# Optimization experiments

Hardware: AMD Instinct MI355X
Metric: run time of the kernel (lower is better)

The kernel has to match this reference:

```python
import jax, jax.numpy as jnp
import numpy as np

LMAX = 8                         # lmax-1 used by s2/so3 irreps
DIMS = [2 * l + 1 for l in range(LMAX + 1)]
S2_OFF = np.cumsum([0] + DIMS).tolist()            # offsets into 81-dim s2 irreps
SO3_OFF = np.cumsum([0] + [d * d for d in DIMS]).tolist()  # offsets into 969-dim so3 irreps
S2_DIM = S2_OFF[-1]              # 81
SO3_DIM = SO3_OFF[-1]            # 969
F_IN = 81                        # multiplicity into S2Conv
F_SO3 = 300
C = 768                          # encoder feature channels
KS = 7                           # encoder feature map / kernel size
B = 8
G_S2 = 48                        # s2 healpix grid rec_level=1
G_ACT = 4096                     # SO3Activation grid points (stand-in for res=20 grid)
G_SO3 = 36864                    # so3 healpix grid rec_level=3


def setup_inputs() -> dict:
    key = jax.random.key(0)
    ks = jax.random.split(key, 7)
    return {
        "x": jax.random.normal(ks[0], (B, C, KS, KS), jnp.float32),
        "F": jax.random.normal(ks[1], (F_IN, S2_DIM * C, KS, KS), jnp.float32) * 0.02,
        "w_s2": jax.random.normal(ks[2], (F_IN, F_SO3, G_S2), jnp.float32) * 0.1,
        "Y": jax.random.normal(ks[3], (G_S2, S2_DIM), jnp.float32),
        "w_so3": jax.random.normal(ks[4], (F_SO3, 1, G_SO3), jnp.float32) * 0.1,
        "D": jax.random.normal(ks[5], (G_SO3, SO3_DIM), jnp.float32),
        "D_act": jax.random.normal(ks[6], (G_ACT, SO3_DIM), jnp.float32),
    }


def _forward(x, F, w_s2, Y, w_so3, D, D_act):
    b = x.shape[0]
    # ---- Induction layer: split expanded R2Conv filter into 768-channel chunks,
    # stack, contract with feature map. g_split: (n=81, c_out=81, C, 7, 7)
    g = jnp.swapaxes(F.reshape(F_IN, S2_DIM, C, KS, KS), 0, 1)
    y = jnp.einsum('ijkhw,akhw->aji', g, x)          # (B, 81, 81): (batch, f_in, s2 irreps)

    # ---- S2Conv: expand kernel into irrep space, per-l block linear (s2 -> so3 irreps)
    psi = jnp.einsum('ni,xyn->xyi', Y, w_s2) / np.sqrt(G_S2)  # (81, 300, 81)
    outs = []
    for l, d in enumerate(DIMS):
        o = S2_OFF[l]
        xl = y[:, :, o:o + d]                        # (B, f_in, 2l+1)
        wl = psi[:, :, o:o + d]                      # (f_in, f_out, mul_out=2l+1)
        ol = jnp.einsum('bfm,fgu->bgum', xl, wl) / np.sqrt(F_IN)
        outs.append(ol.reshape(b, F_SO3, d * d))
    z = jnp.concatenate(outs, axis=-1)               # (B, 300, 969)

    # ---- SO3Activation: to grid, relu, back to irreps
    s = jnp.einsum('bfi,gi->bfg', z, D_act)
    z = jnp.einsum('bfg,gi->bfi', jax.nn.relu(s), D_act) / G_ACT

    # ---- SO3Conv: expand kernel via Wigner-D buffer, per-l block linear (so3 -> so3)
    psi2 = jnp.einsum('ni,xyn->xyi', D, w_so3) / np.sqrt(G_SO3)  # (300, 1, 969)
    outs = []
    for l, d in enumerate(DIMS):
        o = SO3_OFF[l]
        xl = z[:, :, o:o + d * d].reshape(b, F_SO3, d, d)   # (B, f, u, m)
        wl = psi2[:, :, o:o + d * d].reshape(F_SO3, 1, d, d)  # (f, g, v, u)
        ol = jnp.einsum('bfum,fgvu->bgvm', xl, wl) / np.sqrt(F_SO3 * d)
        outs.append(ol.reshape(b, 1, d * d))
    return jnp.concatenate(outs, axis=-1)            # (B, 1, 969)


def reference(x, F, w_s2, Y, w_so3, D, D_act):
    return _forward(x, F, w_s2, Y, w_so3, D, D_act)
```

## Files before the change

kernel.cpp:

```cpp
#include <hip/hip_runtime.h>
#include <hip/hip_bf16.h>
#include <math.h>

#define THREADS 256

constexpr int B_    = 8;
constexpr int C_    = 768;
constexpr int KS_   = 7;
constexpr int F_IN  = 81;
constexpr int F_SO3 = 300;
constexpr int S2_DIM  = 81;
constexpr int SO3_DIM = 969;
constexpr int G_S2  = 48;
constexpr int G_ACT = 4096;
constexpr int G_SO3 = 36864;
constexpr int CKK   = C_ * KS_ * KS_;
constexpr int CKK4  = CKK / 4;
constexpr int NPAIR = F_IN * S2_DIM;

constexpr int D2_SPLIT = 4;
constexpr int E1_SPLIT = 16;
constexpr int F_SPLIT  = 5;

__constant__ int d_S2_OFF[10]  = {0, 1, 4, 9, 16, 25, 36, 49, 64, 81};
__constant__ int d_SO3_OFF[10] = {0, 1, 10, 35, 84, 165, 286, 455, 680, 969};

struct CEnt { unsigned char u, m, so, l; };
struct CLut { CEnt v[992]; };
constexpr CLut make_clut() {
  CLut t{};
  int S2O[10]  = {0, 1, 4, 9, 16, 25, 36, 49, 64, 81};
  int SO3O[10] = {0, 1, 10, 35, 84, 165, 286, 455, 680, 969};
  for (int i = 0; i < 969; ++i) {
    int l = 0;
    while (i >= SO3O[l + 1]) ++l;
    int d = 2 * l + 1, r = i - SO3O[l];
    t.v[i].u  = (unsigned char)(r / d);
    t.v[i].m  = (unsigned char)(r % d);
    t.v[i].so = (unsigned char)S2O[l];
    t.v[i].l  = (unsigned char)l;
  }
  return t;
}
__constant__ CLut g_clut = make_clut();

using short8 = __attribute__((ext_vector_type(8))) short;
using f32x4  = __attribute__((ext_vector_type(4))) float;
using f4v    = __attribute__((ext_vector_type(4))) float;

#define GL16(gp, lp)                                                        \
  __builtin_amdgcn_global_load_lds(                                         \
      (const __attribute__((address_space(1))) void*)(gp),                  \
      (__attribute__((address_space(3))) void*)(lp), 16, 0, 0)

constexpr size_t AL(size_t x) { return (x + 1023) & ~(size_t)1023; }
constexpr size_t O_Y     = 0;
constexpr size_t O_PSI   = O_Y     + AL((size_t)8 * NPAIR * 4);
constexpr size_t O_ZBF   = O_PSI   + AL((size_t)F_IN * F_SO3 * 81 * 4);
constexpr size_t O_DACT  = O_ZBF   + AL((size_t)2432 * 1024 * 2);
constexpr size_t O_DACTT = O_DACT  + AL((size_t)4096 * 1024 * 2);
constexpr size_t O_WSO3  = O_DACTT + AL((size_t)1024 * 4096 * 2);
constexpr size_t O_DT    = O_WSO3  + AL((size_t)384 * 36864 * 2);
constexpr size_t O_SBF   = O_DT    + AL((size_t)1024 * 36864 * 2);
constexpr size_t O_D2P   = O_SBF   + AL((size_t)2432 * 4096 * 2);
constexpr size_t O_E1P   = O_D2P   + AL((size_t)D2_SPLIT * 2432 * 1024 * 4);
constexpr size_t O_PSI2  = O_E1P   + AL((size_t)E1_SPLIT * 384 * 1024 * 4);
constexpr size_t O_SFP   = O_PSI2  + AL((size_t)F_SO3 * SO3_DIM * 4);
constexpr size_t FAST_NEED = O_SFP + AL((size_t)F_SPLIT * 8 * SO3_DIM * 4);

constexpr size_t WS_Y    = 0;
constexpr size_t WS_PSI  = 52488;
constexpr size_t WS_Z    = 2020788;
constexpr size_t WS_S    = 4346388;
constexpr size_t WS_Z2   = 14176788;
constexpr size_t WS_P2P  = 16502388;
constexpr size_t WS_PSI2 = 18827988;

__global__ __launch_bounds__(THREADS) void k_stage_a3(
    const float* __restrict__ Fm, const float* __restrict__ x, float* __restrict__ y) {
  const int p0  = blockIdx.x * 3;
  const int tid = threadIdx.x;
  const f4v* __restrict__ F4 = (const f4v*)Fm;
  const f4v* __restrict__ x4 = (const f4v*)x;

  float acc[3][8];
#pragma unroll
  for (int p = 0; p < 3; ++p)
#pragma unroll
    for (int b = 0; b < 8; ++b) acc[p][b] = 0.f;

  for (int i = tid; i < CKK4; i += THREADS) {
    f4v xv[8];
#pragma unroll
    for (int b = 0; b < 8; ++b) xv[b] = x4[b * CKK4 + i];
#pragma unroll
    for (int p = 0; p < 3; ++p) {
      f4v fv = __builtin_nontemporal_load(&F4[(size_t)(p0 + p) * CKK4 + i]);
#pragma unroll
      for (int b = 0; b < 8; ++b)
        acc[p][b] += fv[0] * xv[b][0] + fv[1] * xv[b][1] + fv[2] * xv[b][2] + fv[3] * xv[b][3];
    }
  }

  __shared__ float red[4][24];
  const int lane = tid & 63, wid = tid >> 6;
#pragma unroll
  for (int p = 0; p < 3; ++p) {
#pragma unroll
    for (int b = 0; b < 8; ++b) {
      float v = acc[p][b];
      v += __shfl_down(v, 32);
      v += __shfl_down(v, 16);
      v += __shfl_down(v, 8);
      v += __shfl_down(v, 4);
      v += __shfl_down(v, 2);
      v += __shfl_down(v, 1);
      if (lane == 0) red[wid][p * 8 + b] = v;
    }
  }
  __syncthreads();
  if (tid < 24) {
    float v = red[0][tid] + red[1][tid] + red[2][tid] + red[3][tid];
    int p = tid / 8, b = tid % 8;
    y[(size_t)b * NPAIR + p0 + p] = v;
  }
}

__device__ __forceinline__ void cvt_body(const float* __restrict__ src,
                                         __hip_bfloat16* __restrict__ dst,
                                         int R, int Cs, int Cp, int blk) {
  size_t idx = (size_t)blk * THREADS + threadIdx.x;
  int r = (int)(idx / (unsigned)Cp), c = (int)(idx % (unsigned)Cp);
  float v = (r < R && c < Cs) ? src[(size_t)r * Cs + c] : 0.f;
  dst[idx] = __float2bfloat16(v);
}

__device__ __forceinline__ void tr_body(const float* __restrict__ src,
                                        __hip_bfloat16* __restrict__ dst,
                                        int R, int Cs, size_t dstStride, int bx, int by) {
  __shared__ float tile[32][33];
  const int c0 = bx * 32, r0 = by * 32;
  const int tx = threadIdx.x & 31, ty = threadIdx.x >> 5;
#pragma unroll
  for (int i = 0; i < 32; i += 8) {
    int r = r0 + ty + i, c = c0 + tx;
    tile[ty + i][tx] = (r < R && c < Cs) ? src[(size_t)r * Cs + c] : 0.f;
  }
  __syncthreads();
#pragma unroll
  for (int i = 0; i < 32; i += 8) {
    int c = c0 + ty + i, r = r0 + tx;
    if (c < Cs && r < R) dst[(size_t)c * dstStride + r] = __float2bfloat16(tile[tx][ty + i]);
  }
}

__device__ __forceinline__ void psi_body(const float* __restrict__ w_s2,
                                         const float* __restrict__ Y,
                                         float* __restrict__ psi, int blk) {
  int idx = blk * THREADS + threadIdx.x;
  if (idx >= F_IN * F_SO3 * S2_DIM) return;
  int s  = idx % S2_DIM;
  int fg = idx / S2_DIM;
  const float* w = w_s2 + (size_t)fg * G_S2;
  float acc = 0.f;
#pragma unroll 8
  for (int n = 0; n < G_S2; ++n) acc += w[n] * Y[n * S2_DIM + s];
  psi[idx] = acc * 0.14433756729740643f;
}

constexpr int UB1 = 16384;
constexpr int UB2 = 3968;
constexpr int UB3 = 55296;
constexpr int UB4 = 35712;
constexpr int UB5 = 7689;
constexpr int UB_TOT = UB1 + UB2 + UB3 + UB4 + UB5;

__global__ __launch_bounds__(THREADS) void k_uber(
    const float* __restrict__ D_act, __hip_bfloat16* __restrict__ Dact_bf,
    __hip_bfloat16* __restrict__ DactT_bf,
    const float* __restrict__ w_so3, __hip_bfloat16* __restrict__ wso3_bf,
    const float* __restrict__ D, __hip_bfloat16* __restrict__ DT_bf,
    const float* __restrict__ w_s2, const float* __restrict__ Y, float* __restrict__ psi) {
  int b = blockIdx.x;
  if (b < UB1) { cvt_body(D_act, Dact_bf, G_ACT, SO3_DIM, 1024, b); return; }
  b -= UB1;
  if (b < UB2) { tr_body(D_act, DactT_bf, G_ACT, SO3_DIM, 4096, b % 31, b / 31); return; }
  b -= UB2;
  if (b < UB3) { cvt_body(w_so3, wso3_bf, F_SO3, G_SO3, G_SO3, b); return; }
  b -= UB3;
  if (b < UB4) { tr_body(D, DT_bf, G_SO3, SO3_DIM, 36864, b % 31, b / 31); return; }
  b -= UB4;
  psi_body(w_s2, Y, psi, b);
}

__global__ __launch_bounds__(THREADS) void k_stage_c_bf(
    const float* __restrict__ y, const float* __restrict__ psi, __hip_bfloat16* __restrict__ z) {
  const int b = blockIdx.x / F_SO3;
  const int g = blockIdx.x % F_SO3;
  __shared__ float ybl[NPAIR];
  __shared__ float psl[NPAIR];
  const int tid = threadIdx.x;
  for (int t = tid; t < NPAIR; t += THREADS) {
    ybl[t] = y[(size_t)b * NPAIR + t];
    int f = t / S2_DIM, s = t % S2_DIM;
    psl[t] = psi[((size_t)f * F_SO3 + g) * S2_DIM + s];
  }
  __syncthreads();
  for (int i = tid; i < 1024; i += THREADS) {
    float acc = 0.f;
    if (i < SO3_DIM) {
      CEnt e = g_clut.v[i];
      int im = e.so + e.m, iu = e.so + e.u;
#pragma unroll 9
      for (int f = 0; f < F_IN; ++f)
        acc += ybl[f * S2_DIM + im] * psl[f * S2_DIM + iu];
      acc *= (1.0f / 9.0f);
    }
    z[((size_t)b * F_SO3 + g) * 1024 + i] = __float2bfloat16(acc);
  }
}

struct GemmDesc {
  const __hip_bfloat16* A;
  const __hip_bfloat16* B;
  void* C;
  int K, kSpan, Ncols;
  float scale;
  size_t splitStride;
  int gx, gy, gz, epi;
};

__device__ __forceinline__ void mfma_nt_body(const GemmDesc g, unsigned lin) {
  __shared__ __align__(16) char smem[32768];
  char* As = smem;
  char* Bs = smem + 16384;

  unsigned nwg = (unsigned)(g.gx * g.gy * g.gz);
  if ((nwg & 7u) == 0u) {
    unsigned q = nwg >> 3;
    lin = (lin & 7u) * q + (lin >> 3);
  }
  const int bxi = (int)(lin % (unsigned)g.gx);
  const unsigned t1 = lin / (unsigned)g.gx;
  const int byi = (int)(t1 % (unsigned)g.gy);
  const int bzi = (int)(t1 / (unsigned)g.gy);

  const int t    = threadIdx.x;
  const int lane = t & 63;
  const int wave = t >> 6;
  const int wr   = wave >> 1, wc = wave & 1;
  const int bm = byi * 128, bn = bxi * 128;
  const int kBegin = bzi * g.kSpan;
  const int kEnd   = kBegin + g.kSpan;

  const char* pA[4];
  const char* pB[4];
  int ldsOff[4];
#pragma unroll
  for (int i = 0; i < 4; ++i) {
    int L   = i * 4096 + t * 16;
    int row = L >> 7;
    int kb  = (L & 127) ^ ((row & 7) << 4);
    pA[i] = (const char*)g.A + ((size_t)(bm + row) * g.K) * 2 + kb;
    pB[i] = (const char*)g.B + ((size_t)(bn + row) * g.K) * 2 + kb;
    ldsOff[i] = L;
  }

  f32x4 acc[4][4] = {};

  for (int k0 = kBegin; k0 < kEnd; k0 += 64) {
    size_t koff = (size_t)k0 * 2;
#pragma unroll
    for (int i = 0; i < 4; ++i) {
      GL16(pA[i] + koff, As + ldsOff[i]);
      GL16(pB[i] + koff, Bs + ldsOff[i]);
    }
    __syncthreads();
#pragma unroll
    for (int kk = 0; kk < 2; ++kk) {
      const int klin = kk * 64 + ((lane >> 4) << 4);
      short8 af[4], bfr[4];
#pragma unroll
      for (int m = 0; m < 4; ++m) {
        int ra = (wr << 6) + (m << 4) + (lane & 15);
        af[m] = *(const short8*)(As + ra * 128 + (klin ^ ((ra & 7) << 4)));
        int rb = (wc << 6) + (m << 4) + (lane & 15);
        bfr[m] = *(const short8*)(Bs + rb * 128 + (klin ^ ((rb & 7) << 4)));
      }
#pragma unroll
      for (int m = 0; m < 4; ++m)
#pragma unroll
        for (int n = 0; n < 4; ++n)
          acc[m][n] = __builtin_amdgcn_mfma_f32_16x16x32_bf16(af[m], bfr[n], acc[m][n], 0, 0, 0);
    }
    __syncthreads();
  }

  const int rbase = bm + (wr << 6) + ((lane >> 4) << 2);
  const int cbase = bn + (wc << 6) + (lane & 15);
  if (g.epi == 0) {
    float* C = (float*)g.C + (size_t)bzi * g.splitStride;
#pragma unroll
    for (int m = 0; m < 4; ++m)
#pragma unroll
      for (int n = 0; n < 4; ++n)
#pragma unroll
        for (int r = 0; r < 4; ++r)
          C[(size_t)(rbase + m * 16 + r) * g.Ncols + (cbase + n * 16)] = acc[m][n][r] * g.scale;
  } else {
    __hip_bfloat16* C = (__hip_bfloat16*)g.C;
#pragma unroll
    for (int m = 0; m < 4; ++m)
#pragma unroll
      for (int n = 0; n < 4; ++n)
#pragma unroll
        for (int r = 0; r < 4; ++r)
          C[(size_t)(rbase + m * 16 + r) * g.Ncols + (cbase + n * 16)] =
              __float2bfloat16(fmaxf(acc[m][n][r], 0.f));
  }
}

__global__ __launch_bounds__(THREADS) void k_mfma_dual(GemmDesc g0, GemmDesc g1, int n0) {
  if ((int)blockIdx.x < n0) mfma_nt_body(g0, blockIdx.x);
  else                      mfma_nt_body(g1, blockIdx.x - n0);
}

__global__ __launch_bounds__(THREADS) void k_mfma_reduce(
    GemmDesc g, int n0,
    const float* __restrict__ parts, float* __restrict__ dst, int R, int C,
    size_t rowStride, size_t splitStride, size_t dstStride, int nSplit, float scale) {
  if ((int)blockIdx.x < n0) { mfma_nt_body(g, blockIdx.x); return; }
  int idx = (int)(blockIdx.x - n0) * THREADS + threadIdx.x;
  if (idx >= R * C) return;
  int r = idx / C, c = idx % C;
  float a = 0.f;
  for (int s = 0; s < nSplit; ++s) a += parts[(size_t)s * splitStride + (size_t)r * rowStride + c];
  dst[(size_t)r * dstStride + c] = a * scale;
}

__global__ __launch_bounds__(THREADS) void k_stage_f_part(
    const float* __restrict__ d2p, const float* __restrict__ psi2, float* __restrict__ partial) {
  const int b  = blockIdx.x / 9;
  const int l  = blockIdx.x % 9;
  const int sp = blockIdx.y;
  const int d = 2 * l + 1, d2 = d * d;
  const int off = d_SO3_OFF[l];
  constexpr size_t SS = (size_t)2432 * 1024;
  __shared__ float zb[10][289];
  __shared__ float pb[10][289];
  const int tid = threadIdx.x;
  float acc[2] = {0.f, 0.f};
  const int fBeg = sp * (F_SO3 / F_SPLIT), fEnd = fBeg + F_SO3 / F_SPLIT;
  for (int fc = fBeg; fc < fEnd; fc += 10) {
    for (int t = tid; t < 10 * d2; t += THREADS) {
      int fl = t / d2, q = t - fl * d2;
      int f  = fc + fl;
      size_t zi = ((size_t)b * F_SO3 + f) * 1024 + off + q;
      float zv = d2p[zi] + d2p[zi + SS] + d2p[zi + 2 * SS] + d2p[zi + 3 * SS];
      zb[fl][q] = zv * (1.0f / G_ACT);
      pb[fl][q] = psi2[(size_t)f * SO3_DIM + off + q];
    }
    __syncthreads();
#pragma unroll 2
    for (int io = 0; io < 2; ++io) {
      int i = tid + io * THREADS;
      if (i < d2) {
        int v = i / d, m = i - v * d;
        float a = acc[io];
#pragma unroll
        for (int fl = 0; fl < 10; ++fl) {
          float s_ = 0.f;
          for (int u = 0; u < d; ++u)
            s_ += zb[fl][u * d + m] * pb[fl][v * d + u];
          a += s_;
        }
        acc[io] = a;
      }
    }
    __syncthreads();
  }
  for (int io = 0; io < 2; ++io) {
    int i = tid + io * THREADS;
    if (i < d2) partial[((size_t)sp * 8 + b) * SO3_DIM + off + i] = acc[io];
  }
}

__global__ __launch_bounds__(THREADS) void k_stage_f_red(
    const float* __restrict__ partial, float* __restrict__ out) {
  int idx = blockIdx.x * THREADS + threadIdx.x;
  if (idx >= 8 * SO3_DIM) return;
  int b = idx / SO3_DIM, i = idx % SO3_DIM;
  int l = g_clut.v[i].l;
  float a = 0.f;
#pragma unroll
  for (int sp = 0; sp < F_SPLIT; ++sp)
    a += partial[((size_t)sp * 8 + b) * SO3_DIM + i];
  out[(size_t)b * SO3_DIM + i] = a * rsqrtf(300.0f * (float)(2 * l + 1));
}

__global__ __launch_bounds__(THREADS) void k_psi(
    const float* __restrict__ w_s2, const float* __restrict__ Y, float* __restrict__ psi) {
  psi_body(w_s2, Y, psi, blockIdx.x);
}

__global__ __launch_bounds__(THREADS) void k_stage_c(
    const float* __restrict__ y, const float* __restrict__ psi, float* __restrict__ z) {
  const int b = blockIdx.x / F_SO3;
  const int g = blockIdx.x % F_SO3;
  __shared__ float ybl[NPAIR];
  __shared__ float psl[NPAIR];
  const int tid = threadIdx.x;
  for (int t = tid; t < NPAIR; t += THREADS) {
    ybl[t] = y[(size_t)b * NPAIR + t];
    int f = t / S2_DIM, s = t % S2_DIM;
    psl[t] = psi[((size_t)f * F_SO3 + g) * S2_DIM + s];
  }
  __syncthreads();
  for (int i = tid; i < SO3_DIM; i += THREADS) {
    CEnt e = g_clut.v[i];
    int im = e.so + e.m, iu = e.so + e.u;
    float acc = 0.f;
#pragma unroll 9
    for (int f = 0; f < F_IN; ++f)
      acc += ybl[f * S2_DIM + im] * psl[f * S2_DIM + iu];
    z[((size_t)b * F_SO3 + g) * SO3_DIM + i] = acc * (1.0f / 9.0f);
  }
}

__global__ __launch_bounds__(THREADS) void k_gemm_nt_relu(
    const float* __restrict__ A, const float* __restrict__ Bm, float* __restrict__ Cm,
    int M, int N, int K) {
  __shared__ float As[16][68];
  __shared__ float Bs[16][68];
  const int bm = blockIdx.y * 64, bn = blockIdx.x * 64;
  const int t  = threadIdx.x;
  const int lk = t & 15, lm = t >> 4;
  const int tn = t & 15, tm = t >> 4;
  float acc[4][4] = {};
  for (int k0 = 0; k0 < K; k0 += 16) {
    int gk = k0 + lk;
#pragma unroll
    for (int j = 0; j < 4; ++j) {
      int m  = lm + 16 * j;
      int gm = bm + m;
      As[lk][m] = (gm < M && gk < K) ? A[(size_t)gm * K + gk] : 0.f;
      int gn = bn + m;
      Bs[lk][m] = (gn < N && gk < K) ? Bm[(size_t)gn * K + gk] : 0.f;
    }
    __syncthreads();
#pragma unroll
    for (int k = 0; k < 16; ++k) {
      float4 av = *(const float4*)&As[k][tm * 4];
      float4 bv = *(const float4*)&Bs[k][tn * 4];
      float a[4] = {av.x, av.y, av.z, av.w};
      float bb[4] = {bv.x, bv.y, bv.z, bv.w};
#pragma unroll
      for (int i2 = 0; i2 < 4; ++i2)
#pragma unroll
        for (int j2 = 0; j2 < 4; ++j2)
          acc[i2][j2] += a[i2] * bb[j2];
    }
    __syncthreads();
  }
#pragma unroll
  for (int i2 = 0; i2 < 4; ++i2) {
    int gm = bm + tm * 4 + i2;
    if (gm >= M) continue;
#pragma unroll
    for (int j2 = 0; j2 < 4; ++j2) {
      int gn = bn + tn * 4 + j2;
      if (gn < N) Cm[(size_t)gm * N + gn] = fmaxf(acc[i2][j2], 0.f);
    }
  }
}

__global__ __launch_bounds__(THREADS) void k_gemm_nn(
    const float* __restrict__ A, const float* __restrict__ Bm, float* __restrict__ Cm,
    int M, int N, int K, int kSpan, float scale, size_t cStride) {
  __shared__ float As[16][68];
  __shared__ float Bs[16][68];
  const int bm = blockIdx.y * 64, bn = blockIdx.x * 64;
  const int t   = threadIdx.x;
  const int lk  = t & 15, lm = t >> 4;
  const int ln  = t & 63, lkq = t >> 6;
  const int tn  = t & 15, tm = t >> 4;
  const int kBegin = blockIdx.z * kSpan;
  const int kEnd   = kBegin + kSpan;
  float* C = Cm + (size_t)blockIdx.z * cStride;
  float acc[4][4] = {};
  for (int k0 = kBegin; k0 < kEnd; k0 += 16) {
    {
      int gk = k0 + lk;
#pragma unroll
      for (int j = 0; j < 4; ++j) {
        int m = lm + 16 * j, gm = bm + m;
        As[lk][m] = (gm < M) ? A[(size_t)gm * K + gk] : 0.f;
      }
    }
    {
      int gn = bn + ln;
#pragma unroll
      for (int j = 0; j < 4; ++j) {
        int k = lkq + 4 * j;
        Bs[k][ln] = (gn < N) ? Bm[(size_t)(k0 + k) * N + gn] : 0.f;
      }
    }
    __syncthreads();
#pragma unroll
    for (int k = 0; k < 16; ++k) {
      float4 av = *(const float4*)&As[k][tm * 4];
      float4 bv = *(const float4*)&Bs[k][tn * 4];
      float a[4] = {av.x, av.y, av.z, av.w};
      float bb[4] = {bv.x, bv.y, bv.z, bv.w};
#pragma unroll
      for (int i2 = 0; i2 < 4; ++i2)
#pragma unroll
        for (int j2 = 0; j2 < 4; ++j2)
          acc[i2][j2] += a[i2] * bb[j2];
    }
    __syncthreads();
  }
#pragma unroll
  for (int i2 = 0; i2 < 4; ++i2) {
    int gm = bm + tm * 4 + i2;
    if (gm >= M) continue;
#pragma unroll
    for (int j2 = 0; j2 < 4; ++j2) {
      int gn = bn + tn * 4 + j2;
      if (gn < N) C[(size_t)gm * N + gn] = acc[i2][j2] * scale;
    }
  }
}

__global__ __launch_bounds__(THREADS) void k_reduce_psi2(
    const float* __restrict__ parts, float* __restrict__ psi2) {
  int idx = blockIdx.x * THREADS + threadIdx.x;
  if (idx >= F_SO3 * SO3_DIM) return;
  float acc = 0.f;
#pragma unroll
  for (int s = 0; s < 8; ++s) acc += parts[(size_t)s * (F_SO3 * SO3_DIM) + idx];
  psi2[idx] = acc * (1.0f / 192.0f);
}

__global__ __launch_bounds__(THREADS) void k_stage_f(
    const float* __restrict__ z2, const float* __restrict__ psi2, float* __restrict__ out,
    int zStride) {
  const int b = blockIdx.x / 9;
  const int l = blockIdx.x % 9;
  const int d = 2 * l + 1, d2 = d * d;
  const int off = d_SO3_OFF[l];
  __shared__ float zb[10][289];
  __shared__ float pb[10][289];
  const int tid = threadIdx.x;
  float acc[2] = {0.f, 0.f};
  const float scale = rsqrtf(300.0f * (float)d);
  for (int fc = 0; fc < F_SO3; fc += 10) {
    for (int t = tid; t < 10 * d2; t += THREADS) {
      int fl = t / d2, q = t - fl * d2;
      int f  = fc + fl;
      zb[fl][q] = z2[((size_t)b * F_SO3 + f) * zStride + off + q];
      pb[fl][q] = psi2[(size_t)f * SO3_DIM + off + q];
    }
    __syncthreads();
#pragma unroll 2
    for (int io = 0; io < 2; ++io) {
      int i = tid + io * THREADS;
      if (i < d2) {
        int v = i / d, m = i - v * d;
        float a = acc[io];
#pragma unroll
        for (int fl = 0; fl < 10; ++fl) {
          float s_ = 0.f;
          for (int u = 0; u < d; ++u)
            s_ += zb[fl][u * d + m] * pb[fl][v * d + u];
          a += s_;
        }
        acc[io] = a;
      }
    }
    __syncthreads();
  }
  for (int io = 0; io < 2; ++io) {
    int i = tid + io * THREADS;
    if (i < d2) out[(size_t)b * SO3_DIM + off + i] = acc[io] * scale;
  }
}

extern "C" void kernel_launch(void* const* d_in, const int* in_sizes, int n_in,
                              void* d_out, int out_size, void* d_ws, size_t ws_size,
                              hipStream_t stream) {
  const float* x     = (const float*)d_in[0];
  const float* Fm    = (const float*)d_in[1];
  const float* w_s2  = (const float*)d_in[2];
  const float* Y     = (const float*)d_in[3];
  const float* w_so3 = (const float*)d_in[4];
  const float* D     = (const float*)d_in[5];
  const float* D_act = (const float*)d_in[6];
  float* out = (float*)d_out;

  if (ws_size >= FAST_NEED) {
    char* p = (char*)d_ws;
    float*          y       = (float*)(p + O_Y);
    float*          psi     = (float*)(p + O_PSI);
    __hip_bfloat16* z_bf    = (__hip_bfloat16*)(p + O_ZBF);
    __hip_bfloat16* Dact_bf = (__hip_bfloat16*)(p + O_DACT);
    __hip_bfloat16* DactT_bf= (__hip_bfloat16*)(p + O_DACTT);
    __hip_bfloat16* wso3_bf = (__hip_bfloat16*)(p + O_WSO3);
    __hip_bfloat16* DT_bf   = (__hip_bfloat16*)(p + O_DT);
    __hip_bfloat16* s_bf    = (__hip_bfloat16*)(p + O_SBF);
    float*          d2p     = (float*)(p + O_D2P);
    float*          e1p     = (float*)(p + O_E1P);
    float*          psi2    = (float*)(p + O_PSI2);
    float*          sfp     = (float*)(p + O_SFP);

    k_stage_a3<<<NPAIR / 3, THREADS, 0, stream>>>(Fm, x, y);
    k_uber<<<UB_TOT, THREADS, 0, stream>>>(
        D_act, Dact_bf, DactT_bf, w_so3, wso3_bf, D, DT_bf, w_s2, Y, psi);
    k_stage_c_bf<<<B_ * F_SO3, THREADS, 0, stream>>>(y, psi, z_bf);

    GemmDesc e1{wso3_bf, DT_bf, e1p, G_SO3, G_SO3 / E1_SPLIT, 1024, 1.f,
                (size_t)384 * 1024, 8, 3, E1_SPLIT, 0};
    GemmDesc d1{z_bf, Dact_bf, s_bf, 1024, 1024, 4096, 1.f, 0, 32, 19, 1, 1};
    int nE1 = 8 * 3 * E1_SPLIT;
    int nD1 = 32 * 19;
    k_mfma_dual<<<nE1 + nD1, THREADS, 0, stream>>>(e1, d1, nE1);

    GemmDesc d2{s_bf, DactT_bf, d2p, 4096, 4096 / D2_SPLIT, 1024, 1.f,
                (size_t)2432 * 1024, 8, 19, D2_SPLIT, 0};
    int nD2 = 8 * 19 * D2_SPLIT;
    int nE1r = (F_SO3 * SO3_DIM + THREADS - 1) / THREADS;
    k_mfma_reduce<<<nD2 + nE1r, THREADS, 0, stream>>>(
        d2, nD2, e1p, psi2, F_SO3, SO3_DIM, 1024, (size_t)384 * 1024, SO3_DIM,
        E1_SPLIT, 1.0f / 192.0f);

    k_stage_f_part<<<dim3(B_ * 9, F_SPLIT), THREADS, 0, stream>>>(d2p, psi2, sfp);
    k_stage_f_red<<<(8 * SO3_DIM + THREADS - 1) / THREADS, THREADS, 0, stream>>>(sfp, out);
  } else {
    float* ws  = (float*)d_ws;
    float* y    = ws + WS_Y;
    float* psi  = ws + WS_PSI;
    float* z    = ws + WS_Z;
    float* s    = ws + WS_S;
    float* z2   = ws + WS_Z2;
    float* p2p  = ws + WS_P2P;
    float* psi2 = ws + WS_PSI2;

    k_stage_a3<<<NPAIR / 3, THREADS, 0, stream>>>(Fm, x, y);
    k_psi<<<(F_IN * F_SO3 * S2_DIM + THREADS - 1) / THREADS, THREADS, 0, stream>>>(w_s2, Y, psi);
    k_stage_c<<<B_ * F_SO3, THREADS, 0, stream>>>(y, psi, z);
    k_gemm_nt_relu<<<dim3(G_ACT / 64, (B_ * F_SO3 + 63) / 64), THREADS, 0, stream>>>(
        z, D_act, s, B_ * F_SO3, G_ACT, SO3_DIM);
    k_gemm_nn<<<dim3((SO3_DIM + 63) / 64, (B_ * F_SO3 + 63) / 64, 1), THREADS, 0, stream>>>(
        s, D_act, z2, B_ * F_SO3, SO3_DIM, G_ACT, G_ACT, 1.0f / G_ACT, 0);
    k_gemm_nn<<<dim3((SO3_DIM + 63) / 64, (F_SO3 + 63) / 64, 8), THREADS, 0, stream>>>(
        w_so3, D, p2p, F_SO3, SO3_DIM, G_SO3, G_SO3 / 8, 1.0f, (size_t)F_SO3 * SO3_DIM);
    k_reduce_psi2<<<(F_SO3 * SO3_DIM + THREADS - 1) / THREADS, THREADS, 0, stream>>>(p2p, psi2);
    k_stage_f<<<B_ * 9, THREADS, 0, stream>>>(z2, psi2, out, SO3_DIM);
  }
}
```

Before: 611.0 us.

## Regroup independent stages into fused launches to overlap stage A, C and GEMMs

```diff
diff --git a/kernel.cpp b/kernel.cpp
--- a/kernel.cpp
+++ b/kernel.cpp
@@ -76,9 +76,10 @@
 constexpr size_t WS_P2P  = 16502388;
 constexpr size_t WS_PSI2 = 18827988;
 
-__global__ __launch_bounds__(THREADS) void k_stage_a3(
-    const float* __restrict__ Fm, const float* __restrict__ x, float* __restrict__ y) {
-  const int p0  = blockIdx.x * 3;
+__device__ __forceinline__ void stage_a_body(
+    const float* __restrict__ Fm, const float* __restrict__ x, float* __restrict__ y,
+    char* smemc, int blk) {
+  const int p0  = blk * 3;
   const int tid = threadIdx.x;
   const f4v* __restrict__ F4 = (const f4v*)Fm;
   const f4v* __restrict__ x4 = (const f4v*)x;
@@ -102,7 +103,7 @@
     }
   }
 
-  __shared__ float red[4][24];
+  float (*red)[24] = (float(*)[24])smemc;
   const int lane = tid & 63, wid = tid >> 6;
 #pragma unroll
   for (int p = 0; p < 3; ++p) {
@@ -137,8 +138,9 @@
 
 __device__ __forceinline__ void tr_body(const float* __restrict__ src,
                                         __hip_bfloat16* __restrict__ dst,
-                                        int R, int Cs, size_t dstStride, int bx, int by) {
-  __shared__ float tile[32][33];
+                                        int R, int Cs, size_t dstStride, int bx, int by,
+                                        char* smemc) {
+  float (*tile)[33] = (float(*)[33])smemc;
   const int c0 = bx * 32, r0 = by * 32;
   const int tx = threadIdx.x & 31, ty = threadIdx.x >> 5;
 #pragma unroll
@@ -168,37 +170,43 @@
   psi[idx] = acc * 0.14433756729740643f;
 }
 
+constexpr int PA  = NPAIR / 3;
 constexpr int UB1 = 16384;
 constexpr int UB2 = 3968;
 constexpr int UB3 = 55296;
 constexpr int UB4 = 35712;
 constexpr int UB5 = 7689;
-constexpr int UB_TOT = UB1 + UB2 + UB3 + UB4 + UB5;
-
-__global__ __launch_bounds__(THREADS) void k_uber(
+constexpr int PREP_TOT = PA + UB1 + UB2 + UB3 + UB4 + UB5;
+
+__global__ __launch_bounds__(THREADS) void k_prep(
+    const float* __restrict__ Fm, const float* __restrict__ x, float* __restrict__ y,
     const float* __restrict__ D_act, __hip_bfloat16* __restrict__ Dact_bf,
     __hip_bfloat16* __restrict__ DactT_bf,
     const float* __restrict__ w_so3, __hip_bfloat16* __restrict__ wso3_bf,
     const float* __restrict__ D, __hip_bfloat16* __restrict__ DT_bf,
     const float* __restrict__ w_s2, const float* __restrict__ Y, float* __restrict__ psi) {
+  __shared__ __align__(16) char smem[4352];
   int b = blockIdx.x;
+  if (b < PA) { stage_a_body(Fm, x, y, smem, b); return; }
+  b -= PA;
   if (b < UB1) { cvt_body(D_act, Dact_bf, G_ACT, SO3_DIM, 1024, b); return; }
   b -= UB1;
-  if (b < UB2) { tr_body(D_act, DactT_bf, G_ACT, SO3_DIM, 4096, b % 31, b / 31); return; }
+  if (b < UB2) { tr_body(D_act, DactT_bf, G_ACT, SO3_DIM, 4096, b % 31, b / 31, smem); return; }
   b -= UB2;
   if (b < UB3) { cvt_body(w_so3, wso3_bf, F_SO3, G_SO3, G_SO3, b); return; }
   b -= UB3;
-  if (b < UB4) { tr_body(D, DT_bf, G_SO3, SO3_DIM, 36864, b % 31, b / 31); return; }
+  if (b < UB4) { tr_body(D, DT_bf, G_SO3, SO3_DIM, 36864, b % 31, b / 31, smem); return; }
   b -= UB4;
   psi_body(w_s2, Y, psi, b);
 }
 
-__global__ __launch_bounds__(THREADS) void k_stage_c_bf(
-    const float* __restrict__ y, const float* __restrict__ psi, __hip_bfloat16* __restrict__ z) {
-  const int b = blockIdx.x / F_SO3;
-  const int g = blockIdx.x % F_SO3;
-  __shared__ float ybl[NPAIR];
-  __shared__ float psl[NPAIR];
+__device__ __forceinline__ void stage_c_body(
+    const float* __restrict__ y, const float* __restrict__ psi, __hip_bfloat16* __restrict__ z,
+    char* smemc, int blk) {
+  const int b = blk / F_SO3;
+  const int g = blk % F_SO3;
+  float* ybl = (float*)smemc;
+  float* psl = ybl + 6592;
   const int tid = threadIdx.x;
   for (int t = tid; t < NPAIR; t += THREADS) {
     ybl[t] = y[(size_t)b * NPAIR + t];
@@ -230,8 +238,7 @@
   int gx, gy, gz, epi;
 };
 
-__device__ __forceinline__ void mfma_nt_body(const GemmDesc g, unsigned lin) {
-  __shared__ __align__(16) char smem[32768];
+__device__ __forceinline__ void mfma_nt_body(const GemmDesc g, unsigned lin, char* smem) {
   char* As = smem;
   char* Bs = smem + 16384;
 
@@ -320,22 +327,31 @@
   }
 }
 
-__global__ __launch_bounds__(THREADS) void k_mfma_dual(GemmDesc g0, GemmDesc g1, int n0) {
-  if ((int)blockIdx.x < n0) mfma_nt_body(g0, blockIdx.x);
-  else                      mfma_nt_body(g1, blockIdx.x - n0);
-}
-
-__global__ __launch_bounds__(THREADS) void k_mfma_reduce(
-    GemmDesc g, int n0,
+__global__ __launch_bounds__(THREADS) void k_e1_c(
+    GemmDesc e1, int nE1,
+    const float* __restrict__ y, const float* __restrict__ psi, __hip_bfloat16* __restrict__ z) {
+  __shared__ __align__(16) char smem[52672];
+  if ((int)blockIdx.x < nE1) mfma_nt_body(e1, blockIdx.x, smem);
+  else                       stage_c_body(y, psi, z, smem, blockIdx.x - nE1);
+}
+
+__global__ __launch_bounds__(THREADS) void k_d1_e1r(
+    GemmDesc d1, int n0,
     const float* __restrict__ parts, float* __restrict__ dst, int R, int C,
     size_t rowStride, size_t splitStride, size_t dstStride, int nSplit, float scale) {
-  if ((int)blockIdx.x < n0) { mfma_nt_body(g, blockIdx.x); return; }
+  __shared__ __align__(16) char smem[32768];
+  if ((int)blockIdx.x < n0) { mfma_nt_body(d1, blockIdx.x, smem); return; }
   int idx = (int)(blockIdx.x - n0) * THREADS + threadIdx.x;
   if (idx >= R * C) return;
   int r = idx / C, c = idx % C;
   float a = 0.f;
   for (int s = 0; s < nSplit; ++s) a += parts[(size_t)s * splitStride + (size_t)r * rowStride + c];
   dst[(size_t)r * dstStride + c] = a * scale;
+}
+
+__global__ __launch_bounds__(THREADS) void k_mfma_single(GemmDesc g) {
+  __shared__ __align__(16) char smem[32768];
+  mfma_nt_body(g, blockIdx.x, smem);
 }
 
 __global__ __launch_bounds__(THREADS) void k_stage_f_part(
@@ -398,6 +414,12 @@
   out[(size_t)b * SO3_DIM + i] = a * rsqrtf(300.0f * (float)(2 * l + 1));
 }
 
+__global__ __launch_bounds__(THREADS) void k_stage_a3(
+    const float* __restrict__ Fm, const float* __restrict__ x, float* __restrict__ y) {
+  __shared__ __align__(16) char smem[512];
+  stage_a_body(Fm, x, y, smem, blockIdx.x);
+}
+
 __global__ __launch_bounds__(THREADS) void k_psi(
     const float* __restrict__ w_s2, const float* __restrict__ Y, float* __restrict__ psi) {
   psi_body(w_s2, Y, psi, blockIdx.x);
@@ -613,25 +635,24 @@
     float*          psi2    = (float*)(p + O_PSI2);
     float*          sfp     = (float*)(p + O_SFP);
 
-    k_stage_a3<<<NPAIR / 3, THREADS, 0, stream>>>(Fm, x, y);
-    k_uber<<<UB_TOT, THREADS, 0, stream>>>(
-        D_act, Dact_bf, DactT_bf, w_so3, wso3_bf, D, DT_bf, w_s2, Y, psi);
-    k_stage_c_bf<<<B_ * F_SO3, THREADS, 0, stream>>>(y, psi, z_bf);
+    k_prep<<<PREP_TOT, THREADS, 0, stream>>>(
+        Fm, x, y, D_act, Dact_bf, DactT_bf, w_so3, wso3_bf, D, DT_bf, w_s2, Y, psi);
 
     GemmDesc e1{wso3_bf, DT_bf, e1p, G_SO3, G_SO3 / E1_SPLIT, 1024, 1.f,
                 (size_t)384 * 1024, 8, 3, E1_SPLIT, 0};
+    int nE1 = 8 * 3 * E1_SPLIT;
+    k_e1_c<<<nE1 + B_ * F_SO3, THREADS, 0, stream>>>(e1, nE1, y, psi, z_bf);
+
     GemmDesc d1{z_bf, Dact_bf, s_bf, 1024, 1024, 4096, 1.f, 0, 32, 19, 1, 1};
-    int nE1 = 8 * 3 * E1_SPLIT;
     int nD1 = 32 * 19;
-    k_mfma_dual<<<nE1 + nD1, THREADS, 0, stream>>>(e1, d1, nE1);
+    int nE1r = (F_SO3 * SO3_DIM + THREADS - 1) / THREADS;
+    k_d1_e1r<<<nD1 + nE1r, THREADS, 0, stream>>>(
+        d1, nD1, e1p, psi2, F_SO3, SO3_DIM, 1024, (size_t)384 * 1024, SO3_DIM,
+        E1_SPLIT, 1.0f / 192.0f);
 
     GemmDesc d2{s_bf, DactT_bf, d2p, 4096, 4096 / D2_SPLIT, 1024, 1.f,
                 (size_t)2432 * 1024, 8, 19, D2_SPLIT, 0};
-    int nD2 = 8 * 19 * D2_SPLIT;
-    int nE1r = (F_SO3 * SO3_DIM + THREADS - 1) / THREADS;
-    k_mfma_reduce<<<nD2 + nE1r, THREADS, 0, stream>>>(
-        d2, nD2, e1p, psi2, F_SO3, SO3_DIM, 1024, (size_t)384 * 1024, SO3_DIM,
-        E1_SPLIT, 1.0f / 192.0f);
+    k_mfma_single<<<8 * 19 * D2_SPLIT, THREADS, 0, stream>>>(d2);
 
     k_stage_f_part<<<dim3(B_ * 9, F_SPLIT), THREADS, 0, stream>>>(d2p, psi2, sfp);
     k_stage_f_red<<<(8 * SO3_DIM + THREADS - 1) / THREADS, THREADS, 0, stream>>>(sfp, out);
```

New measurement: 640.1 us. 4.8% more time.
